# Kernel optimization log

Measured on AMD Instinct MI355X. Metric: run time of the kernel, lower is better.

Reference implementation:

```python
import jax, jax.numpy as jnp
import numpy as np

TEMPERATURE = 8.0   # sqrt(d_k), d_k = 64
TOP_K = 5           # SparseAttention default top_k in mimicry/RIMs
EPS = 1e-7          # matches torch 10e-8


def _sparsify(attn_rows):
    """Per-row top-k sparsification: keep mass above the k-th largest value,
    clamp at zero, renormalize. attn_rows: [N, L]."""
    topk_vals = jax.lax.top_k(attn_rows, TOP_K)[0]          # [N, K]
    delta = topk_vals[:, -1:] + EPS                          # k-th largest per row
    w = jnp.maximum(attn_rows - delta, 0.0)                  # clamp(min=0)
    return w / (jnp.sum(w, axis=1, keepdims=True) + EPS)


def setup_inputs() -> dict:
    key = jax.random.key(0)
    kq, kk, kv = jax.random.split(key, 3)
    B, L, D = 4, 4096, 64
    q = jax.random.normal(kq, (B, L, D), dtype=jnp.float32)
    k = jax.random.normal(kk, (B, L, D), dtype=jnp.float32)
    v = jax.random.normal(kv, (B, L, D), dtype=jnp.float32)
    return {"q": q, "k": k, "v": v}


def reference(q, k, v):
    # attn = softmax(q k^T / temperature); dropout is identity in eval mode
    attn = jnp.einsum('bqd,bkd->bqk', q / TEMPERATURE, k)   # [B, Lq, Lk]
    attn = jax.nn.softmax(attn, axis=-1)
    B, Lq, Lk = attn.shape
    attn = _sparsify(attn.reshape(B * Lq, Lk)).reshape(B, Lq, Lk)
    out = jnp.einsum('bqk,bkd->bqd', attn, v)               # [B, Lq, Dv]
    return out, attn
```

## Files before the change

kernel.cpp:

```cpp
#include <hip/hip_runtime.h>
#include <math.h>

#define NB 4
#define L 4096
#define D 64
#define WS_QL 1048576
#define WS_K  2097152
#define KBS   524288
#define KPL   262144
#define QSCALE 0.1803368801111243f

typedef __attribute__((ext_vector_type(8))) short short8;
typedef __attribute__((ext_vector_type(4))) float floatx4;

static __device__ inline ushort2 f2bf2(float x) {
    unsigned int u = __builtin_bit_cast(unsigned int, x);
    unsigned int uh = u + (0x7FFFu + ((u >> 16) & 1u));
    unsigned short h = (unsigned short)(uh >> 16);
    float hf = __builtin_bit_cast(float, (unsigned int)h << 16);
    float r = x - hf;
    unsigned int v = __builtin_bit_cast(unsigned int, r);
    unsigned short l = (unsigned short)((v + (0x7FFFu + ((v >> 16) & 1u))) >> 16);
    ushort2 p; p.x = h; p.y = l; return p;
}

__global__ __launch_bounds__(256)
void convert_kernel(const float* __restrict__ qg, const float* __restrict__ kg,
                    unsigned short* __restrict__ ws) {
    unsigned int i = blockIdx.x * 256 + threadIdx.x;
    if (i < 262144) {
        float4 qv = ((const float4*)qg)[i];
        ushort2 p0 = f2bf2(qv.x * QSCALE), p1 = f2bf2(qv.y * QSCALE),
                p2 = f2bf2(qv.z * QSCALE), p3 = f2bf2(qv.w * QSCALE);
        ushort4 h; h.x = p0.x; h.y = p1.x; h.z = p2.x; h.w = p3.x;
        ushort4 l; l.x = p0.y; l.y = p1.y; l.z = p2.y; l.w = p3.y;
        *(ushort4*)&ws[i * 4] = h;
        *(ushort4*)&ws[WS_QL + i * 4] = l;
    } else {
        unsigned int j = i - 262144;
        float4 kv = ((const float4*)kg)[j];
        ushort2 p0 = f2bf2(kv.x), p1 = f2bf2(kv.y), p2 = f2bf2(kv.z), p3 = f2bf2(kv.w);
        ushort4 h; h.x = p0.x; h.y = p1.x; h.z = p2.x; h.w = p3.x;
        ushort4 l; l.x = p0.y; l.y = p1.y; l.z = p2.y; l.w = p3.y;
        unsigned int bcol = j >> 4;
        unsigned int f4   = j & 15;
        unsigned int b    = bcol >> 12, col = bcol & 4095;
        unsigned int cq   = f4 >> 1, half = f4 & 1;
        size_t base = WS_K + (size_t)b * KBS + ((size_t)cq * 4096 + col) * 8 + half * 4;
        *(ushort4*)&ws[base] = h;
        *(ushort4*)&ws[base + KPL] = l;
    }
}

#define SENT 0x7FFFFFFF

__global__ __launch_bounds__(256, 4)
void sparse_attn_kernel(const unsigned short* __restrict__ ws,
                        const float* __restrict__ vg,
                        float* __restrict__ outg) {
    __shared__ float smv[3][16][5];
    __shared__ int   smc[3][16][4];

    const int tid  = threadIdx.x;
    const int lane = tid & 63;
    const int wid  = tid >> 6;
    const int c16  = lane & 15;
    const int quad = lane >> 4;

    const int sblk  = (blockIdx.x & 7) * 128 + (blockIdx.x >> 3);
    const int qbase = sblk * 16;
    const int b     = qbase >> 12;

    const unsigned short* qh   = ws;
    const unsigned short* ql   = ws + WS_QL;
    const unsigned short* kbat = ws + WS_K + (size_t)b * KBS;
    const float* vb = vg + (size_t)b * L * D;
    float* attng = outg + (size_t)NB * L * D;

    const int qrow = qbase + c16;
    const short8 a0h = *(const short8*)&qh[(size_t)qrow * 64 + quad * 8];
    const short8 a1h = *(const short8*)&qh[(size_t)qrow * 64 + 32 + quad * 8];
    const short8 a0l = *(const short8*)&ql[(size_t)qrow * 64 + quad * 8];
    const short8 a1l = *(const short8*)&ql[(size_t)qrow * 64 + 32 + quad * 8];

    float tv[4][5];
    int   tc[4][4];
#pragma unroll
    for (int r = 0; r < 4; ++r) {
#pragma unroll
        for (int i = 0; i < 5; ++i) tv[r][i] = -INFINITY;
#pragma unroll
        for (int i = 0; i < 4; ++i) tc[r][i] = SENT;
    }

    const int colq = wid * 1024;
    const unsigned short* bp0 = kbat + ((size_t)(quad)     * 4096 + colq + c16) * 8;
    const unsigned short* bp1 = kbat + ((size_t)(4 + quad) * 4096 + colq + c16) * 8;
    const float4 zv = make_float4(0.f, 0.f, 0.f, 0.f);

#pragma unroll 4
    for (int cg = 0; cg < 64; ++cg) {
        const int off = cg * 128;
        short8 b0h = *(const short8*)(bp0 + off);
        short8 b1h = *(const short8*)(bp1 + off);
        short8 b0l = *(const short8*)(bp0 + KPL + off);
        short8 b1l = *(const short8*)(bp1 + KPL + off);
        floatx4 acc = {0.f, 0.f, 0.f, 0.f};
        acc = __builtin_amdgcn_mfma_f32_16x16x32_bf16(a0h, b0h, acc, 0, 0, 0);
        acc = __builtin_amdgcn_mfma_f32_16x16x32_bf16(a1h, b1h, acc, 0, 0, 0);
        acc = __builtin_amdgcn_mfma_f32_16x16x32_bf16(a0l, b0h, acc, 0, 0, 0);
        acc = __builtin_amdgcn_mfma_f32_16x16x32_bf16(a1l, b1h, acc, 0, 0, 0);
        acc = __builtin_amdgcn_mfma_f32_16x16x32_bf16(a0h, b0l, acc, 0, 0, 0);
        acc = __builtin_amdgcn_mfma_f32_16x16x32_bf16(a1h, b1l, acc, 0, 0, 0);

        {
            int idx = cg * 64 + lane;
            *(float4*)&attng[(size_t)(qbase + (idx >> 8)) * L + colq + (idx & 255) * 4] = zv;
        }

        const int col = colq + cg * 16 + c16;
#pragma unroll
        for (int r = 0; r < 4; ++r) {
            float s = acc[r];
            bool q0 = s > tv[r][0];
            bool q1 = s > tv[r][1];
            bool q2 = s > tv[r][2];
            bool q3 = s > tv[r][3];
            bool q4 = s > tv[r][4];
            tv[r][4] = q4 ? (q3 ? tv[r][3] : s)   : tv[r][4];
            tv[r][3] = q3 ? (q2 ? tv[r][2] : s)   : tv[r][3];
            tc[r][3] = q3 ? (q2 ? tc[r][2] : col) : tc[r][3];
            tv[r][2] = q2 ? (q1 ? tv[r][1] : s)   : tv[r][2];
            tc[r][2] = q2 ? (q1 ? tc[r][1] : col) : tc[r][2];
            tv[r][1] = q1 ? (q0 ? tv[r][0] : s)   : tv[r][1];
            tc[r][1] = q1 ? (q0 ? tc[r][0] : col) : tc[r][1];
            tv[r][0] = q0 ? s   : tv[r][0];
            tc[r][0] = q0 ? col : tc[r][0];
        }
    }

    float gv[4][5]; int gc[4][4];
#pragma unroll
    for (int r = 0; r < 4; ++r) {
#pragma unroll
        for (int k5 = 0; k5 < 4; ++k5) {
            float cv = tv[r][0]; int cc = tc[r][0];
#pragma unroll
            for (int m = 8; m >= 1; m >>= 1) {
                float ov = __shfl_xor(cv, m, 64);
                int   oc = __shfl_xor(cc, m, 64);
                if (ov > cv || (ov == cv && oc < cc)) { cv = ov; cc = oc; }
            }
            gv[r][k5] = cv; gc[r][k5] = cc;
            if (tc[r][0] == cc && tv[r][0] == cv) {
                tv[r][0] = tv[r][1]; tc[r][0] = tc[r][1];
                tv[r][1] = tv[r][2]; tc[r][1] = tc[r][2];
                tv[r][2] = tv[r][3]; tc[r][2] = tc[r][3];
                tv[r][3] = tv[r][4]; tc[r][3] = SENT;
                tv[r][4] = -INFINITY;
            }
        }
        float fv = tv[r][0];
#pragma unroll
        for (int m = 8; m >= 1; m >>= 1) fv = fmaxf(fv, __shfl_xor(fv, m, 64));
        gv[r][4] = fv;
    }

    if (wid > 0) {
#pragma unroll
        for (int r = 0; r < 4; ++r) {
            const int rowl = quad * 4 + r;
            if (c16 < 4) {
                smv[wid - 1][rowl][c16] = gv[r][c16];
                smc[wid - 1][rowl][c16] = gc[r][c16];
            } else if (c16 == 4) {
                smv[wid - 1][rowl][4] = gv[r][4];
            }
        }
    }
    __syncthreads();

    if (wid == 0) {
#pragma unroll
        for (int r = 0; r < 4; ++r) {
            const int rowl = quad * 4 + r;
            float lv[5]; int lc[4];
#pragma unroll
            for (int i = 0; i < 5; ++i) lv[i] = gv[r][i];
#pragma unroll
            for (int i = 0; i < 4; ++i) lc[i] = gc[r][i];

#pragma unroll
            for (int f = 0; f < 3; ++f) {
#pragma unroll
                for (int s5 = 0; s5 < 4; ++s5) {
                    float v = smv[f][rowl][s5];
                    int   c = smc[f][rowl][s5];
                    bool q0 = v > lv[0];
                    bool q1 = v > lv[1];
                    bool q2 = v > lv[2];
                    bool q3 = v > lv[3];
                    bool q4 = v > lv[4];
                    lv[4] = q4 ? (q3 ? lv[3] : v) : lv[4];
                    lv[3] = q3 ? (q2 ? lv[2] : v) : lv[3];
                    lc[3] = q3 ? (q2 ? lc[2] : c) : lc[3];
                    lv[2] = q2 ? (q1 ? lv[1] : v) : lv[2];
                    lc[2] = q2 ? (q1 ? lc[1] : c) : lc[2];
                    lv[1] = q1 ? (q0 ? lv[0] : v) : lv[1];
                    lc[1] = q1 ? (q0 ? lc[0] : c) : lc[1];
                    lv[0] = q0 ? v : lv[0];
                    lc[0] = q0 ? c : lc[0];
                }
                {
                    float v = smv[f][rowl][4];
                    bool q0 = v > lv[0];
                    bool q1 = v > lv[1];
                    bool q2 = v > lv[2];
                    bool q3 = v > lv[3];
                    bool q4 = v > lv[4];
                    lv[4] = q4 ? (q3 ? lv[3] : v) : lv[4];
                    lv[3] = q3 ? (q2 ? lv[2] : v) : lv[3];
                    lv[2] = q2 ? (q1 ? lv[1] : v) : lv[2];
                    lv[1] = q1 ? (q0 ? lv[0] : v) : lv[1];
                    lv[0] = q0 ? v : lv[0];
                }
            }

            float u0 = exp2f(lv[0] - lv[4]) - 1.0f;
            float u1 = exp2f(lv[1] - lv[4]) - 1.0f;
            float u2 = exp2f(lv[2] - lv[4]) - 1.0f;
            float u3 = exp2f(lv[3] - lv[4]) - 1.0f;
            float inv = 1.0f / (u0 + u1 + u2 + u3 + 1e-30f);
            float w0 = u0 * inv, w1 = u1 * inv, w2 = u2 * inv, w3 = u3 * inv;

            const int rowabs = qbase + rowl;

            unsigned int i0 = min((unsigned)lc[0], 4095u);
            unsigned int i1 = min((unsigned)lc[1], 4095u);
            unsigned int i2 = min((unsigned)lc[2], 4095u);
            unsigned int i3 = min((unsigned)lc[3], 4095u);
            const float4 v0 = *(const float4*)(vb + (size_t)i0 * D + c16 * 4);
            const float4 v1 = *(const float4*)(vb + (size_t)i1 * D + c16 * 4);
            const float4 v2 = *(const float4*)(vb + (size_t)i2 * D + c16 * 4);
            const float4 v3 = *(const float4*)(vb + (size_t)i3 * D + c16 * 4);
            float4 o;
            o.x = w0 * v0.x + w1 * v1.x + w2 * v2.x + w3 * v3.x;
            o.y = w0 * v0.y + w1 * v1.y + w2 * v2.y + w3 * v3.y;
            o.z = w0 * v0.z + w1 * v1.z + w2 * v2.z + w3 * v3.z;
            o.w = w0 * v0.w + w1 * v1.w + w2 * v2.w + w3 * v3.w;
            *(float4*)(outg + (size_t)rowabs * D + c16 * 4) = o;

            if (c16 < 4) {
                float wv = c16 == 0 ? w0 : c16 == 1 ? w1 : c16 == 2 ? w2 : w3;
                int   cs = c16 == 0 ? lc[0] : c16 == 1 ? lc[1]
                         : c16 == 2 ? lc[2] : lc[3];
                if ((unsigned)cs < 4096u && wv > 0.f)
                    attng[(size_t)rowabs * L + cs] = wv;
            }
        }
    }
}

extern "C" void kernel_launch(void* const* d_in, const int* in_sizes, int n_in,
                              void* d_out, int out_size, void* d_ws, size_t ws_size,
                              hipStream_t stream) {
    const float* q = (const float*)d_in[0];
    const float* k = (const float*)d_in[1];
    const float* v = (const float*)d_in[2];
    float* out = (float*)d_out;
    unsigned short* ws = (unsigned short*)d_ws;

    convert_kernel<<<2048, 256, 0, stream>>>(q, k, ws);

    sparse_attn_kernel<<<1024, 256, 0, stream>>>(ws, v, out);
}
```

Baseline: 334.0 us.

## Pack column index into score low bits and use med3 top-5 insertion

Column indices are encoded into the low 12 mantissa bits of each score, so the per-row top-5 tracking is a pure float network built from fmax/fmed3 instead of compare-and-select chains over separate value and index arrays. The cross-lane reduction becomes a shuffle-and-merge of whole sorted lists, replacing four sequential argmax rounds, and the shared-memory index array goes away. This cuts VALU and register work in the hot loop. The cost is that scores lose 12 mantissa bits, which can change tie-breaking and perturb the sparse weights slightly.

```diff
diff --git a/kernel.cpp b/kernel.cpp
--- a/kernel.cpp
+++ b/kernel.cpp
@@ -52,14 +52,35 @@
     }
 }
 
-#define SENT 0x7FFFFFFF
+static __device__ inline void ins5(float d[5], float t) {
+    float n0 = fmaxf(d[0], t);
+    float n1 = __builtin_amdgcn_fmed3f(t, d[0], d[1]);
+    float n2 = __builtin_amdgcn_fmed3f(t, d[1], d[2]);
+    float n3 = __builtin_amdgcn_fmed3f(t, d[2], d[3]);
+    float n4 = __builtin_amdgcn_fmed3f(t, d[3], d[4]);
+    d[0] = n0; d[1] = n1; d[2] = n2; d[3] = n3; d[4] = n4;
+}
+
+static __device__ inline void merge5(float d[5], const float o[5]) {
+#pragma unroll
+    for (int j = 0; j < 5; ++j) {
+        float t = o[j];
+        float carry = d[j];
+        d[j] = fmaxf(d[j], t);
+#pragma unroll
+        for (int k = j + 1; k < 5; ++k) {
+            float pk = d[k];
+            d[k] = __builtin_amdgcn_fmed3f(t, carry, d[k]);
+            carry = pk;
+        }
+    }
+}
 
 __global__ __launch_bounds__(256, 4)
 void sparse_attn_kernel(const unsigned short* __restrict__ ws,
                         const float* __restrict__ vg,
                         float* __restrict__ outg) {
     __shared__ float smv[3][16][5];
-    __shared__ int   smc[3][16][4];
 
     const int tid  = threadIdx.x;
     const int lane = tid & 63;
@@ -84,16 +105,13 @@
     const short8 a1l = *(const short8*)&ql[(size_t)qrow * 64 + 32 + quad * 8];
 
     float tv[4][5];
-    int   tc[4][4];
-#pragma unroll
-    for (int r = 0; r < 4; ++r) {
+#pragma unroll
+    for (int r = 0; r < 4; ++r)
 #pragma unroll
         for (int i = 0; i < 5; ++i) tv[r][i] = -INFINITY;
-#pragma unroll
-        for (int i = 0; i < 4; ++i) tc[r][i] = SENT;
-    }
 
     const int colq = wid * 1024;
+    const int colbase = colq + c16;
     const unsigned short* bp0 = kbat + ((size_t)(quad)     * 4096 + colq + c16) * 8;
     const unsigned short* bp1 = kbat + ((size_t)(4 + quad) * 4096 + colq + c16) * 8;
     const float4 zv = make_float4(0.f, 0.f, 0.f, 0.f);
@@ -118,64 +136,32 @@
             *(float4*)&attng[(size_t)(qbase + (idx >> 8)) * L + colq + (idx & 255) * 4] = zv;
         }
 
-        const int col = colq + cg * 16 + c16;
+        const int cx = (colbase + cg * 16) ^ 4095;
 #pragma unroll
         for (int r = 0; r < 4; ++r) {
-            float s = acc[r];
-            bool q0 = s > tv[r][0];
-            bool q1 = s > tv[r][1];
-            bool q2 = s > tv[r][2];
-            bool q3 = s > tv[r][3];
-            bool q4 = s > tv[r][4];
-            tv[r][4] = q4 ? (q3 ? tv[r][3] : s)   : tv[r][4];
-            tv[r][3] = q3 ? (q2 ? tv[r][2] : s)   : tv[r][3];
-            tc[r][3] = q3 ? (q2 ? tc[r][2] : col) : tc[r][3];
-            tv[r][2] = q2 ? (q1 ? tv[r][1] : s)   : tv[r][2];
-            tc[r][2] = q2 ? (q1 ? tc[r][1] : col) : tc[r][2];
-            tv[r][1] = q1 ? (q0 ? tv[r][0] : s)   : tv[r][1];
-            tc[r][1] = q1 ? (q0 ? tc[r][0] : col) : tc[r][1];
-            tv[r][0] = q0 ? s   : tv[r][0];
-            tc[r][0] = q0 ? col : tc[r][0];
-        }
-    }
-
-    float gv[4][5]; int gc[4][4];
+            int si  = __builtin_bit_cast(int, (float)acc[r]);
+            int tag = cx ^ ((si >> 31) & 4095);
+            int ti  = (si & 0xFFFFF000) | tag;
+            ins5(tv[r], __builtin_bit_cast(float, ti));
+        }
+    }
+
 #pragma unroll
     for (int r = 0; r < 4; ++r) {
 #pragma unroll
-        for (int k5 = 0; k5 < 4; ++k5) {
-            float cv = tv[r][0]; int cc = tc[r][0];
-#pragma unroll
-            for (int m = 8; m >= 1; m >>= 1) {
-                float ov = __shfl_xor(cv, m, 64);
-                int   oc = __shfl_xor(cc, m, 64);
-                if (ov > cv || (ov == cv && oc < cc)) { cv = ov; cc = oc; }
-            }
-            gv[r][k5] = cv; gc[r][k5] = cc;
-            if (tc[r][0] == cc && tv[r][0] == cv) {
-                tv[r][0] = tv[r][1]; tc[r][0] = tc[r][1];
-                tv[r][1] = tv[r][2]; tc[r][1] = tc[r][2];
-                tv[r][2] = tv[r][3]; tc[r][2] = tc[r][3];
-                tv[r][3] = tv[r][4]; tc[r][3] = SENT;
-                tv[r][4] = -INFINITY;
-            }
-        }
-        float fv = tv[r][0];
-#pragma unroll
-        for (int m = 8; m >= 1; m >>= 1) fv = fmaxf(fv, __shfl_xor(fv, m, 64));
-        gv[r][4] = fv;
+        for (int m = 8; m >= 1; m >>= 1) {
+            float o[5];
+#pragma unroll
+            for (int i = 0; i < 5; ++i) o[i] = __shfl_xor(tv[r][i], m, 64);
+            merge5(tv[r], o);
+        }
     }
 
     if (wid > 0) {
 #pragma unroll
         for (int r = 0; r < 4; ++r) {
             const int rowl = quad * 4 + r;
-            if (c16 < 4) {
-                smv[wid - 1][rowl][c16] = gv[r][c16];
-                smc[wid - 1][rowl][c16] = gc[r][c16];
-            } else if (c16 == 4) {
-                smv[wid - 1][rowl][4] = gv[r][4];
-            }
+            if (c16 < 5) smv[wid - 1][rowl][c16] = tv[r][c16];
         }
     }
     __syncthreads();
@@ -184,47 +170,25 @@
 #pragma unroll
         for (int r = 0; r < 4; ++r) {
             const int rowl = quad * 4 + r;
-            float lv[5]; int lc[4];
-#pragma unroll
-            for (int i = 0; i < 5; ++i) lv[i] = gv[r][i];
-#pragma unroll
-            for (int i = 0; i < 4; ++i) lc[i] = gc[r][i];
-
+            float lv[5];
+#pragma unroll
+            for (int i = 0; i < 5; ++i) lv[i] = tv[r][i];
 #pragma unroll
             for (int f = 0; f < 3; ++f) {
-#pragma unroll
-                for (int s5 = 0; s5 < 4; ++s5) {
-                    float v = smv[f][rowl][s5];
-                    int   c = smc[f][rowl][s5];
-                    bool q0 = v > lv[0];
-                    bool q1 = v > lv[1];
-                    bool q2 = v > lv[2];
-                    bool q3 = v > lv[3];
-                    bool q4 = v > lv[4];
-                    lv[4] = q4 ? (q3 ? lv[3] : v) : lv[4];
-                    lv[3] = q3 ? (q2 ? lv[2] : v) : lv[3];
-                    lc[3] = q3 ? (q2 ? lc[2] : c) : lc[3];
-                    lv[2] = q2 ? (q1 ? lv[1] : v) : lv[2];
-                    lc[2] = q2 ? (q1 ? lc[1] : c) : lc[2];
-                    lv[1] = q1 ? (q0 ? lv[0] : v) : lv[1];
-                    lc[1] = q1 ? (q0 ? lc[0] : c) : lc[1];
-                    lv[0] = q0 ? v : lv[0];
-                    lc[0] = q0 ? c : lc[0];
-                }
-                {
-                    float v = smv[f][rowl][4];
-                    bool q0 = v > lv[0];
-                    bool q1 = v > lv[1];
-                    bool q2 = v > lv[2];
-                    bool q3 = v > lv[3];
-                    bool q4 = v > lv[4];
-                    lv[4] = q4 ? (q3 ? lv[3] : v) : lv[4];
-                    lv[3] = q3 ? (q2 ? lv[2] : v) : lv[3];
-                    lv[2] = q2 ? (q1 ? lv[1] : v) : lv[2];
-                    lv[1] = q1 ? (q0 ? lv[0] : v) : lv[1];
-                    lv[0] = q0 ? v : lv[0];
-                }
+                float o[5];
+#pragma unroll
+                for (int i = 0; i < 5; ++i) o[i] = smv[f][rowl][i];
+                merge5(lv, o);
             }
+
+            int t0 = __builtin_bit_cast(int, lv[0]);
+            int t1 = __builtin_bit_cast(int, lv[1]);
+            int t2 = __builtin_bit_cast(int, lv[2]);
+            int t3 = __builtin_bit_cast(int, lv[3]);
+            unsigned int i0 = (unsigned)((t0 & 4095) ^ (t0 >= 0 ? 4095 : 0));
+            unsigned int i1 = (unsigned)((t1 & 4095) ^ (t1 >= 0 ? 4095 : 0));
+            unsigned int i2 = (unsigned)((t2 & 4095) ^ (t2 >= 0 ? 4095 : 0));
+            unsigned int i3 = (unsigned)((t3 & 4095) ^ (t3 >= 0 ? 4095 : 0));
 
             float u0 = exp2f(lv[0] - lv[4]) - 1.0f;
             float u1 = exp2f(lv[1] - lv[4]) - 1.0f;
@@ -235,10 +199,6 @@
 
             const int rowabs = qbase + rowl;
 
-            unsigned int i0 = min((unsigned)lc[0], 4095u);
-            unsigned int i1 = min((unsigned)lc[1], 4095u);
-            unsigned int i2 = min((unsigned)lc[2], 4095u);
-            unsigned int i3 = min((unsigned)lc[3], 4095u);
             const float4 v0 = *(const float4*)(vb + (size_t)i0 * D + c16 * 4);
             const float4 v1 = *(const float4*)(vb + (size_t)i1 * D + c16 * 4);
             const float4 v2 = *(const float4*)(vb + (size_t)i2 * D + c16 * 4);
@@ -252,9 +212,9 @@
 
             if (c16 < 4) {
                 float wv = c16 == 0 ? w0 : c16 == 1 ? w1 : c16 == 2 ? w2 : w3;
-                int   cs = c16 == 0 ? lc[0] : c16 == 1 ? lc[1]
-                         : c16 == 2 ? lc[2] : lc[3];
-                if ((unsigned)cs < 4096u && wv > 0.f)
+                unsigned int cs = c16 == 0 ? i0 : c16 == 1 ? i1
+                                : c16 == 2 ? i2 : i3;
+                if (wv > 0.f)
                     attng[(size_t)rowabs * L + cs] = wv;
             }
         }
```

After: 310.2 us. 7.1% less time.
